# Kernel optimization log

Hardware: AMD Instinct MI355X
Metric: run time of the kernel (lower is better)

## Reference

```python
import jax, jax.numpy as jnp
import numpy as np

D_MODEL = 1024
NUM_HEADS = 16
HEAD_DIM = D_MODEL // NUM_HEADS
B, S = 2, 2048


def setup_inputs() -> dict:
    key = jax.random.key(0)
    ks = jax.random.split(key, 5)
    x = jax.random.normal(ks[0], (B, S, D_MODEL), dtype=jnp.float32)
    # nn.Linear weights are [out_features, in_features]
    Wq = jax.random.normal(ks[1], (D_MODEL, D_MODEL), dtype=jnp.float32) / np.sqrt(D_MODEL)
    Wk = jax.random.normal(ks[2], (HEAD_DIM, D_MODEL), dtype=jnp.float32) / np.sqrt(D_MODEL)
    Wv = jax.random.normal(ks[3], (HEAD_DIM, D_MODEL), dtype=jnp.float32) / np.sqrt(D_MODEL)
    Wo = jax.random.normal(ks[4], (D_MODEL, D_MODEL), dtype=jnp.float32) / np.sqrt(D_MODEL)
    # causal mask, broadcastable to [B, H, S, S]; mask==0 positions get -inf
    mask = jnp.tril(jnp.ones((S, S), dtype=bool))[None, None]
    return {"x": x, "Wq": Wq, "Wk": Wk, "Wv": Wv, "Wo": Wo, "mask": mask}


def reference(x, Wq, Wk, Wv, Wo, mask):
    Bsz, Sl, D = x.shape
    H, hd = NUM_HEADS, HEAD_DIM
    q = (x @ Wq.T).reshape(Bsz, Sl, H, hd)          # [B,S,H,hd]
    k = x @ Wk.T                                    # [B,S,hd] (single shared KV head)
    v = x @ Wv.T                                    # [B,S,hd]
    scale = 1.0 / np.sqrt(hd).astype(np.float32)
    # scores: [B,H,S,S] — full O(n^2) matrix, as in the original module
    scores = jnp.einsum('bshd,btd->bhst', q, k) * scale
    scores = jnp.where(mask, scores, -jnp.inf)
    attn = jax.nn.softmax(scores, axis=-1)
    out = jnp.einsum('bhst,btd->bshd', attn, v).reshape(Bsz, Sl, D)
    return out @ Wo.T
```

## Files before the change

kernel.cpp:

```cpp
#include <hip/hip_runtime.h>
#include <hip/hip_bf16.h>
#include <math.h>

#define BB 2
#define SS 2048
#define DD 1024
#define NH 16
#define HD 64
#define MM (BB * SS)

#define BK 64
#define BKF 32

typedef __hip_bfloat16 bf16;
typedef __bf16 bf16_t;
typedef __attribute__((ext_vector_type(8))) __bf16 bf16x8;
typedef __attribute__((ext_vector_type(4))) __bf16 bf16x4;
typedef __attribute__((ext_vector_type(4))) float floatx4;

#define SCALEQ 0.18033688011112042f

__device__ __forceinline__ int bf16_plausible(unsigned int w) {
    unsigned int bits = (w & 0xFFFFu) << 16;
    float v = __uint_as_float(bits);
    float av = fabsf(v);
    return (av == 0.f || (av >= 9.5367431640625e-7f && av <= 64.f)) ? 1 : 0;
}

__global__ void detect_dtype(const unsigned int* __restrict__ x, int* __restrict__ flag) {
    const int tid = threadIdx.x;
    int good = 0;
    for (int i = tid; i < 256; i += 64) good += bf16_plausible(x[i]);
#pragma unroll
    for (int s = 1; s < 64; s <<= 1) good += __shfl_xor(good, s);
    if (tid == 0) { flag[0] = (good >= 240) ? 0 : 1; flag[1] = 0; }
}

__device__ __forceinline__ void conv_seg(const void* __restrict__ in,
                                         bf16_t* __restrict__ out,
                                         int n, int f, int tid, int T) {
    if (f) {
        const float* p = (const float*)in;
        for (int i = tid * 8; i < n; i += T * 8) {
            float4 a = *(const float4*)(p + i);
            float4 b = *(const float4*)(p + i + 4);
            bf16x8 o;
            o[0] = (bf16_t)a.x; o[1] = (bf16_t)a.y; o[2] = (bf16_t)a.z; o[3] = (bf16_t)a.w;
            o[4] = (bf16_t)b.x; o[5] = (bf16_t)b.y; o[6] = (bf16_t)b.z; o[7] = (bf16_t)b.w;
            *(bf16x8*)(out + i) = o;
        }
    } else {
        const bf16_t* p = (const bf16_t*)in;
        for (int i = tid * 8; i < n; i += T * 8)
            *(bf16x8*)(out + i) = *(const bf16x8*)(p + i);
    }
}

__global__ __launch_bounds__(256) void conv_all(const void* __restrict__ x,
                                                const void* __restrict__ wq,
                                                const void* __restrict__ wk,
                                                const void* __restrict__ wv,
                                                const void* __restrict__ wo,
                                                bf16_t* __restrict__ xb,
                                                bf16_t* __restrict__ wqb,
                                                bf16_t* __restrict__ wkb,
                                                bf16_t* __restrict__ wvb,
                                                bf16_t* __restrict__ wob,
                                                int* __restrict__ flag) {
    __shared__ int goodw[4];
    const int ltid = threadIdx.x;
    int g = bf16_plausible(((const unsigned int*)x)[ltid]);
#pragma unroll
    for (int s = 1; s < 64; s <<= 1) g += __shfl_xor(g, s);
    if ((ltid & 63) == 0) goodw[ltid >> 6] = g;
    __syncthreads();
    const int good = goodw[0] + goodw[1] + goodw[2] + goodw[3];
    const int f = (good >= 240) ? 0 : 1;
    if (blockIdx.x == 0 && ltid == 0) { flag[0] = f; flag[1] = 0; }

    const int tid = blockIdx.x * blockDim.x + ltid;
    const int T = gridDim.x * blockDim.x;
    conv_seg(x, xb, MM * DD, f, tid, T);
    conv_seg(wq, wqb, DD * DD, f, tid, T);
    conv_seg(wk, wkb, HD * DD, f, tid, T);
    conv_seg(wv, wvb, HD * DD, f, tid, T);
    conv_seg(wo, wob, DD * DD, f, tid, T);
}

#define KP2 72

__global__ __launch_bounds__(512) void proj_qkv_b(const bf16_t* __restrict__ X,
                                                  const bf16_t* __restrict__ Wq,
                                                  const bf16_t* __restrict__ Wk,
                                                  const bf16_t* __restrict__ Wv,
                                                  bf16_t* __restrict__ QA,
                                                  bf16_t* __restrict__ Kp,
                                                  bf16_t* __restrict__ VpT) {
    __shared__ bf16_t As[128 * KP2];
    __shared__ bf16_t Bs[128 * KP2];

    const int tid = threadIdx.x;
    const int wave = tid >> 6, lane = tid & 63;
    const int lo = lane & 15, quad = lane >> 4;
    const int wr = wave >> 2, wc = wave & 3;
    const int rowBase = blockIdx.x * 128;
    const int cb = blockIdx.y;

    const int rS = tid >> 2;
    const int c16 = (tid & 3) * 16;

    const bf16_t* arow = X + (size_t)(rowBase + rS) * DD + c16;
    const bf16_t* wrow;
    if (cb < 8)       wrow = Wq + (size_t)(cb * 128 + rS) * DD + c16;
    else if (rS < 64) wrow = Wk + (size_t)rS * DD + c16;
    else              wrow = Wv + (size_t)(rS - 64) * DD + c16;

    floatx4 acc[4][2];
#pragma unroll
    for (int i = 0; i < 4; i++)
#pragma unroll
        for (int j = 0; j < 2; j++) acc[i][j] = (floatx4){0.f, 0.f, 0.f, 0.f};

    bf16x8 aR0[2], bR0[2], aR1[2], bR1[2];
#pragma unroll
    for (int p = 0; p < 2; p++) {
        aR0[p] = *(const bf16x8*)(arow + p * 8);
        bR0[p] = *(const bf16x8*)(wrow + p * 8);
        aR1[p] = *(const bf16x8*)(arow + BK + p * 8);
        bR1[p] = *(const bf16x8*)(wrow + BK + p * 8);
    }

    for (int k0 = 0; k0 < DD; k0 += 2 * BK) {
        __syncthreads();
#pragma unroll
        for (int p = 0; p < 2; p++) {
            *(bf16x8*)&As[rS * KP2 + c16 + p * 8] = aR0[p];
            *(bf16x8*)&Bs[rS * KP2 + c16 + p * 8] = bR0[p];
        }
        __syncthreads();
        if (k0 + 2 * BK < DD) {
#pragma unroll
            for (int p = 0; p < 2; p++) {
                aR0[p] = *(const bf16x8*)(arow + k0 + 2 * BK + p * 8);
                bR0[p] = *(const bf16x8*)(wrow + k0 + 2 * BK + p * 8);
            }
        }
#pragma unroll
        for (int kk = 0; kk < 2; kk++) {
            bf16x8 afr[4], bfr[2];
#pragma unroll
            for (int i = 0; i < 4; i++)
                afr[i] = *(const bf16x8*)&As[(wr * 64 + i * 16 + lo) * KP2 + kk * 32 + quad * 8];
#pragma unroll
            for (int j = 0; j < 2; j++)
                bfr[j] = *(const bf16x8*)&Bs[(wc * 32 + j * 16 + lo) * KP2 + kk * 32 + quad * 8];
#pragma unroll
            for (int i = 0; i < 4; i++)
#pragma unroll
                for (int j = 0; j < 2; j++)
                    acc[i][j] = __builtin_amdgcn_mfma_f32_16x16x32_bf16(afr[i], bfr[j], acc[i][j], 0, 0, 0);
        }
        __syncthreads();
#pragma unroll
        for (int p = 0; p < 2; p++) {
            *(bf16x8*)&As[rS * KP2 + c16 + p * 8] = aR1[p];
            *(bf16x8*)&Bs[rS * KP2 + c16 + p * 8] = bR1[p];
        }
        __syncthreads();
        if (k0 + 3 * BK < DD) {
#pragma unroll
            for (int p = 0; p < 2; p++) {
                aR1[p] = *(const bf16x8*)(arow + k0 + 3 * BK + p * 8);
                bR1[p] = *(const bf16x8*)(wrow + k0 + 3 * BK + p * 8);
            }
        }
#pragma unroll
        for (int kk = 0; kk < 2; kk++) {
            bf16x8 afr[4], bfr[2];
#pragma unroll
            for (int i = 0; i < 4; i++)
                afr[i] = *(const bf16x8*)&As[(wr * 64 + i * 16 + lo) * KP2 + kk * 32 + quad * 8];
#pragma unroll
            for (int j = 0; j < 2; j++)
                bfr[j] = *(const bf16x8*)&Bs[(wc * 32 + j * 16 + lo) * KP2 + kk * 32 + quad * 8];
#pragma unroll
            for (int i = 0; i < 4; i++)
#pragma unroll
                for (int j = 0; j < 2; j++)
                    acc[i][j] = __builtin_amdgcn_mfma_f32_16x16x32_bf16(afr[i], bfr[j], acc[i][j], 0, 0, 0);
        }
    }

#pragma unroll
    for (int i = 0; i < 4; i++)
#pragma unroll
        for (int j = 0; j < 2; j++)
#pragma unroll
            for (int reg = 0; reg < 4; reg++) {
                int row = rowBase + wr * 64 + i * 16 + quad * 4 + reg;
                int c = wc * 32 + j * 16 + lo;
                float v = acc[i][j][reg];
                if (cb < 8) {
                    QA[(size_t)row * DD + cb * 128 + c] = (bf16_t)(v * SCALEQ);
                } else if (c < 64) {
                    Kp[(size_t)row * HD + c] = (bf16_t)v;
                } else {
                    VpT[((size_t)(row >> 11) * HD + (c - 64)) * SS + (row & (SS - 1))] = (bf16_t)v;
                }
            }
}

__global__ __launch_bounds__(512) void proj_o_b(const bf16_t* __restrict__ AO,
                                                const bf16_t* __restrict__ Wo,
                                                void* __restrict__ Cout,
                                                const int* __restrict__ flagOut) {
    const int fout = *flagOut;

    __shared__ bf16_t As[128 * KP2];
    __shared__ bf16_t Bs[128 * KP2];

    const int tid = threadIdx.x;
    const int wave = tid >> 6, lane = tid & 63;
    const int lo = lane & 15, quad = lane >> 4;
    const int wr = wave >> 2, wc = wave & 3;
    const int rowBase = blockIdx.x * 128;
    const int colBase = blockIdx.y * 128;

    const int rS = tid >> 2;
    const int c16 = (tid & 3) * 16;

    const bf16_t* arow = AO + (size_t)(rowBase + rS) * DD + c16;
    const bf16_t* wrow = Wo + (size_t)(colBase + rS) * DD + c16;

    floatx4 acc[4][2];
#pragma unroll
    for (int i = 0; i < 4; i++)
#pragma unroll
        for (int j = 0; j < 2; j++) acc[i][j] = (floatx4){0.f, 0.f, 0.f, 0.f};

    bf16x8 aR0[2], bR0[2], aR1[2], bR1[2];
#pragma unroll
    for (int p = 0; p < 2; p++) {
        aR0[p] = *(const bf16x8*)(arow + p * 8);
        bR0[p] = *(const bf16x8*)(wrow + p * 8);
        aR1[p] = *(const bf16x8*)(arow + BK + p * 8);
        bR1[p] = *(const bf16x8*)(wrow + BK + p * 8);
    }

    for (int k0 = 0; k0 < DD; k0 += 2 * BK) {
        __syncthreads();
#pragma unroll
        for (int p = 0; p < 2; p++) {
            *(bf16x8*)&As[rS * KP2 + c16 + p * 8] = aR0[p];
            *(bf16x8*)&Bs[rS * KP2 + c16 + p * 8] = bR0[p];
        }
        __syncthreads();
        if (k0 + 2 * BK < DD) {
#pragma unroll
            for (int p = 0; p < 2; p++) {
                aR0[p] = *(const bf16x8*)(arow + k0 + 2 * BK + p * 8);
                bR0[p] = *(const bf16x8*)(wrow + k0 + 2 * BK + p * 8);
            }
        }
#pragma unroll
        for (int kk = 0; kk < 2; kk++) {
            bf16x8 afr[4], bfr[2];
#pragma unroll
            for (int i = 0; i < 4; i++)
                afr[i] = *(const bf16x8*)&As[(wr * 64 + i * 16 + lo) * KP2 + kk * 32 + quad * 8];
#pragma unroll
            for (int j = 0; j < 2; j++)
                bfr[j] = *(const bf16x8*)&Bs[(wc * 32 + j * 16 + lo) * KP2 + kk * 32 + quad * 8];
#pragma unroll
            for (int i = 0; i < 4; i++)
#pragma unroll
                for (int j = 0; j < 2; j++)
                    acc[i][j] = __builtin_amdgcn_mfma_f32_16x16x32_bf16(afr[i], bfr[j], acc[i][j], 0, 0, 0);
        }
        __syncthreads();
#pragma unroll
        for (int p = 0; p < 2; p++) {
            *(bf16x8*)&As[rS * KP2 + c16 + p * 8] = aR1[p];
            *(bf16x8*)&Bs[rS * KP2 + c16 + p * 8] = bR1[p];
        }
        __syncthreads();
        if (k0 + 3 * BK < DD) {
#pragma unroll
            for (int p = 0; p < 2; p++) {
                aR1[p] = *(const bf16x8*)(arow + k0 + 3 * BK + p * 8);
                bR1[p] = *(const bf16x8*)(wrow + k0 + 3 * BK + p * 8);
            }
        }
#pragma unroll
        for (int kk = 0; kk < 2; kk++) {
            bf16x8 afr[4], bfr[2];
#pragma unroll
            for (int i = 0; i < 4; i++)
                afr[i] = *(const bf16x8*)&As[(wr * 64 + i * 16 + lo) * KP2 + kk * 32 + quad * 8];
#pragma unroll
            for (int j = 0; j < 2; j++)
                bfr[j] = *(const bf16x8*)&Bs[(wc * 32 + j * 16 + lo) * KP2 + kk * 32 + quad * 8];
#pragma unroll
            for (int i = 0; i < 4; i++)
#pragma unroll
                for (int j = 0; j < 2; j++)
                    acc[i][j] = __builtin_amdgcn_mfma_f32_16x16x32_bf16(afr[i], bfr[j], acc[i][j], 0, 0, 0);
        }
    }

#pragma unroll
    for (int i = 0; i < 4; i++)
#pragma unroll
        for (int j = 0; j < 2; j++)
#pragma unroll
            for (int reg = 0; reg < 4; reg++) {
                int row = rowBase + wr * 64 + i * 16 + quad * 4 + reg;
                int col = colBase + wc * 32 + j * 16 + lo;
                size_t idx = (size_t)row * DD + col;
                if (fout) ((float*)Cout)[idx] = acc[i][j][reg];
                else      ((bf16_t*)Cout)[idx] = (bf16_t)acc[i][j][reg];
            }
}

#define KP 40

__device__ __forceinline__ bf16x8 ld8(const void* p, int f, size_t idx) {
    if (f) {
        const float* q = (const float*)p + idx;
        float4 a = *(const float4*)(q);
        float4 b = *(const float4*)(q + 4);
        bf16x8 o;
        o[0] = (bf16_t)a.x; o[1] = (bf16_t)a.y; o[2] = (bf16_t)a.z; o[3] = (bf16_t)a.w;
        o[4] = (bf16_t)b.x; o[5] = (bf16_t)b.y; o[6] = (bf16_t)b.z; o[7] = (bf16_t)b.w;
        return o;
    }
    return *(const bf16x8*)((const bf16_t*)p + idx);
}

__global__ __launch_bounds__(256) void proj_qkv_f(const void* __restrict__ X,
                                                  const void* __restrict__ Wq,
                                                  const void* __restrict__ Wk,
                                                  const void* __restrict__ Wv,
                                                  bf16_t* __restrict__ QA,
                                                  bf16_t* __restrict__ Kp,
                                                  bf16_t* __restrict__ VpT,
                                                  const int* __restrict__ flag) {
    const int f = *flag;
    __shared__ bf16_t As[64 * KP];
    __shared__ bf16_t Bs[64 * KP];

    const int tid = threadIdx.x;
    const int wave = tid >> 6, lane = tid & 63;
    const int lo = lane & 15, quad = lane >> 4;
    const int wr = wave >> 1, wc = wave & 1;
    const int rowBase = blockIdx.x * 64;
    const int cb = blockIdx.y;

    const int rS = tid >> 2;
    const int c8 = (tid & 3) * 8;

    size_t aidx = (size_t)(rowBase + rS) * DD + c8;
    size_t widx;
    const void* Wsrc;
    if (cb < 16)       { Wsrc = Wq; widx = (size_t)(cb * 64 + rS) * DD + c8; }
    else if (cb == 16) { Wsrc = Wk; widx = (size_t)rS * DD + c8; }
    else               { Wsrc = Wv; widx = (size_t)rS * DD + c8; }

    floatx4 acc[2][2];
#pragma unroll
    for (int i = 0; i < 2; i++)
#pragma unroll
        for (int j = 0; j < 2; j++) acc[i][j] = (floatx4){0.f, 0.f, 0.f, 0.f};

    for (int k0 = 0; k0 < DD; k0 += BKF) {
        __syncthreads();
        *(bf16x8*)&As[rS * KP + c8] = ld8(X, f, aidx + k0);
        *(bf16x8*)&Bs[rS * KP + c8] = ld8(Wsrc, f, widx + k0);
        __syncthreads();
        bf16x8 afr[2], bfr[2];
#pragma unroll
        for (int i = 0; i < 2; i++)
            afr[i] = *(const bf16x8*)&As[(wr * 32 + i * 16 + lo) * KP + quad * 8];
#pragma unroll
        for (int j = 0; j < 2; j++)
            bfr[j] = *(const bf16x8*)&Bs[(wc * 32 + j * 16 + lo) * KP + quad * 8];
#pragma unroll
        for (int i = 0; i < 2; i++)
#pragma unroll
            for (int j = 0; j < 2; j++)
                acc[i][j] = __builtin_amdgcn_mfma_f32_16x16x32_bf16(afr[i], bfr[j], acc[i][j], 0, 0, 0);
    }

#pragma unroll
    for (int i = 0; i < 2; i++)
#pragma unroll
        for (int j = 0; j < 2; j++)
#pragma unroll
            for (int reg = 0; reg < 4; reg++) {
                int row = rowBase + wr * 32 + i * 16 + quad * 4 + reg;
                int c = wc * 32 + j * 16 + lo;
                float v = acc[i][j][reg];
                if (cb < 16) {
                    QA[(size_t)row * DD + cb * 64 + c] = (bf16_t)(v * SCALEQ);
                } else if (cb == 16) {
                    Kp[(size_t)row * HD + c] = (bf16_t)v;
                } else {
                    VpT[((size_t)(row >> 11) * HD + c) * SS + (row & (SS - 1))] = (bf16_t)v;
                }
            }
}

__global__ __launch_bounds__(256) void proj_o_f(const bf16_t* __restrict__ AO,
                                                const void* __restrict__ Wo,
                                                void* __restrict__ Cout,
                                                const int* __restrict__ flagW,
                                                const int* __restrict__ flagOut) {
    const int f = *flagW;
    const int fout = *flagOut;
    __shared__ bf16_t As[64 * KP];
    __shared__ bf16_t Bs[64 * KP];

    const int tid = threadIdx.x;
    const int wave = tid >> 6, lane = tid & 63;
    const int lo = lane & 15, quad = lane >> 4;
    const int wr = wave >> 1, wc = wave & 1;
    const int rowBase = blockIdx.x * 64;
    const int colBase = blockIdx.y * 64;

    const int rS = tid >> 2;
    const int c8 = (tid & 3) * 8;

    size_t aidx = (size_t)(rowBase + rS) * DD + c8;
    size_t widx = (size_t)(colBase + rS) * DD + c8;

    floatx4 acc[2][2];
#pragma unroll
    for (int i = 0; i < 2; i++)
#pragma unroll
        for (int j = 0; j < 2; j++) acc[i][j] = (floatx4){0.f, 0.f, 0.f, 0.f};

    for (int k0 = 0; k0 < DD; k0 += BKF) {
        __syncthreads();
        *(bf16x8*)&As[rS * KP + c8] = *(const bf16x8*)(AO + aidx + k0);
        *(bf16x8*)&Bs[rS * KP + c8] = ld8(Wo, f, widx + k0);
        __syncthreads();
        bf16x8 afr[2], bfr[2];
#pragma unroll
        for (int i = 0; i < 2; i++)
            afr[i] = *(const bf16x8*)&As[(wr * 32 + i * 16 + lo) * KP + quad * 8];
#pragma unroll
        for (int j = 0; j < 2; j++)
            bfr[j] = *(const bf16x8*)&Bs[(wc * 32 + j * 16 + lo) * KP + quad * 8];
#pragma unroll
        for (int i = 0; i < 2; i++)
#pragma unroll
            for (int j = 0; j < 2; j++)
                acc[i][j] = __builtin_amdgcn_mfma_f32_16x16x32_bf16(afr[i], bfr[j], acc[i][j], 0, 0, 0);
    }

#pragma unroll
    for (int i = 0; i < 2; i++)
#pragma unroll
        for (int j = 0; j < 2; j++)
#pragma unroll
            for (int reg = 0; reg < 4; reg++) {
                int row = rowBase + wr * 32 + i * 16 + quad * 4 + reg;
                int col = colBase + wc * 32 + j * 16 + lo;
                size_t idx = (size_t)row * DD + col;
                if (fout) ((float*)Cout)[idx] = acc[i][j][reg];
                else      ((bf16_t*)Cout)[idx] = (bf16_t)acc[i][j][reg];
            }
}

#define PSTR 40
#define DMTHR 8.0f

__global__ __launch_bounds__(512, 4) void attn_mfma(const bf16_t* Q,
                                                    const bf16_t* __restrict__ K,
                                                    const bf16_t* __restrict__ Vt,
                                                    bf16_t* O) {
    const int h = blockIdx.y, b = blockIdx.z;
    const int tid = threadIdx.x;
    const int wq = tid >> 6, lane = tid & 63;
    const int lo = lane & 15, quad = lane >> 4;
    const int x = blockIdx.x;

    const int nA = x + 1;
    int na = 1, bestc = 0x7fffffff;
#pragma unroll
    for (int a = 1; a <= 7; ++a) {
        int cA = (nA + a - 1) / a;
        int cB = (65 - nA + (7 - a)) / (8 - a);
        int c = cA > cB ? cA : cB;
        if (c < bestc) { bestc = c; na = a; }
    }
    int qt, pos, gs;
    if (wq < na) { qt = x;      pos = wq;      gs = na; }
    else         { qt = 63 - x; pos = wq - na; gs = 8 - na; }
    const int q0 = qt * 32;
    const int n = qt + 1;
    const int itS = (n * pos) / gs;
    const int itE = (n * (pos + 1)) / gs;

    __shared__ __align__(16) char smem[4 * 32 * 64 * 4];
    __shared__ float MrgML[4][2][2][16];
    bf16_t* Pw = (bf16_t*)smem + wq * (32 * PSTR);
    float (*MrgO)[32 * 64] = (float (*)[32 * 64])smem;

    bf16x8 qf[2][2];
#pragma unroll
    for (int s = 0; s < 2; s++)
#pragma unroll
        for (int hf = 0; hf < 2; hf++)
            qf[s][hf] = *(const bf16x8*)(Q + ((size_t)(b * SS + q0 + s * 16 + lo)) * DD +
                                         h * HD + hf * 32 + quad * 8);

    floatx4 Oacc[2][4];
    float m_i[2], l_ln[2];
#pragma unroll
    for (int s = 0; s < 2; s++) {
#pragma unroll
        for (int dt = 0; dt < 4; dt++) Oacc[s][dt] = (floatx4){0.f, 0.f, 0.f, 0.f};
        m_i[s] = -1e30f; l_ln[s] = 0.f;
    }

    const bf16_t* Kb = K + (size_t)b * SS * HD;
    const bf16_t* Vb = Vt + (size_t)b * HD * SS;

    if (itS < itE) {
        bf16x8 kf[2][2];
#pragma unroll
        for (int kt = 0; kt < 2; kt++)
#pragma unroll
            for (int hf = 0; hf < 2; hf++)
                kf[kt][hf] = *(const bf16x8*)(Kb + (size_t)(itS * 32 + kt * 16 + lo) * HD +
                                              hf * 32 + quad * 8);

        for (int it = itS; it < itE; it++) {
            const int t0 = it * 32;

            bf16x8 vf[4];
#pragma unroll
            for (int dt = 0; dt < 4; dt++)
                vf[dt] = *(const bf16x8*)(Vb + (size_t)(dt * 16 + lo) * SS + t0 + quad * 8);

            bf16x8 kn[2][2];
            if (it + 1 < itE) {
#pragma unroll
                for (int kt = 0; kt < 2; kt++)
#pragma unroll
                    for (int hf = 0; hf < 2; hf++)
                        kn[kt][hf] = *(const bf16x8*)(Kb + (size_t)(t0 + 32 + kt * 16 + lo) * HD +
                                                      hf * 32 + quad * 8);
            }

            floatx4 st[2][2];
#pragma unroll
            for (int s = 0; s < 2; s++)
#pragma unroll
                for (int kt = 0; kt < 2; kt++) {
                    floatx4 z = (floatx4){0.f, 0.f, 0.f, 0.f};
                    z = __builtin_amdgcn_mfma_f32_16x16x32_bf16(kf[kt][0], qf[s][0], z, 0, 0, 0);
                    z = __builtin_amdgcn_mfma_f32_16x16x32_bf16(kf[kt][1], qf[s][1], z, 0, 0, 0);
                    st[s][kt] = z;
                }

            if (it == qt) {
#pragma unroll
                for (int s = 0; s < 2; s++) {
                    int q = q0 + s * 16 + lo;
#pragma unroll
                    for (int kt = 0; kt < 2; kt++)
#pragma unroll
                        for (int reg = 0; reg < 4; reg++)
                            if (t0 + kt * 16 + quad * 4 + reg > q) st[s][kt][reg] = -1e30f;
                }
            }

#pragma unroll
            for (int s = 0; s < 2; s++) {
                float lm = fmaxf(fmaxf(fmaxf(st[s][0][0], st[s][0][1]), fmaxf(st[s][0][2], st[s][0][3])),
                                 fmaxf(fmaxf(st[s][1][0], st[s][1][1]), fmaxf(st[s][1][2], st[s][1][3])));
                if (__any(lm > m_i[s] + DMTHR)) {
                    float mx = fmaxf(lm, __shfl_xor(lm, 16));
                    mx = fmaxf(mx, __shfl_xor(mx, 32));
                    float mn = fmaxf(m_i[s], mx);
                    float al = exp2f(m_i[s] - mn);
                    m_i[s] = mn;
                    l_ln[s] *= al;
#pragma unroll
                    for (int dt = 0; dt < 4; dt++) Oacc[s][dt] *= al;
                }
                float p[2][4];
#pragma unroll
                for (int kt = 0; kt < 2; kt++)
#pragma unroll
                    for (int reg = 0; reg < 4; reg++)
                        p[kt][reg] = exp2f(st[s][kt][reg] - m_i[s]);
                l_ln[s] += ((p[0][0] + p[0][1]) + (p[0][2] + p[0][3])) +
                           ((p[1][0] + p[1][1]) + (p[1][2] + p[1][3]));
#pragma unroll
                for (int kt = 0; kt < 2; kt++) {
                    bf16x4 pk;
#pragma unroll
                    for (int reg = 0; reg < 4; reg++) pk[reg] = (bf16_t)p[kt][reg];
                    *(bf16x4*)&Pw[(s * 16 + lo) * PSTR + kt * 16 + quad * 4] = pk;
                }
            }

            asm volatile("s_waitcnt lgkmcnt(0)" ::: "memory");

            bf16x8 pb[2];
#pragma unroll
            for (int s = 0; s < 2; s++)
                pb[s] = *(const bf16x8*)&Pw[(s * 16 + lo) * PSTR + quad * 8];
#pragma unroll
            for (int s = 0; s < 2; s++)
#pragma unroll
                for (int dt = 0; dt < 4; dt++)
                    Oacc[s][dt] = __builtin_amdgcn_mfma_f32_16x16x32_bf16(vf[dt], pb[s], Oacc[s][dt], 0, 0, 0);

#pragma unroll
            for (int kt = 0; kt < 2; kt++)
#pragma unroll
                for (int hf = 0; hf < 2; hf++) kf[kt][hf] = kn[kt][hf];
        }
    }

    float l_i[2];
#pragma unroll
    for (int s = 0; s < 2; s++) {
        float l = l_ln[s];
        l += __shfl_xor(l, 16);
        l += __shfl_xor(l, 32);
        l_i[s] = l;
    }

    for (int step = 1; step < 8; step <<= 1) {
        const bool pub = (pos & (2 * step - 1)) == step;
        const bool cmb = ((pos & (2 * step - 1)) == 0) && (pos + step < gs);
        __syncthreads();
        if (pub) {
            float* Ob = MrgO[wq >> 1];
#pragma unroll
            for (int s = 0; s < 2; s++) {
#pragma unroll
                for (int dt = 0; dt < 4; dt++)
#pragma unroll
                    for (int reg = 0; reg < 4; reg++)
                        Ob[(s * 16 + dt * 4 + reg) * 64 + lane] = Oacc[s][dt][reg];
                if (quad == 0) {
                    MrgML[wq >> 1][s][0][lo] = m_i[s];
                    MrgML[wq >> 1][s][1][lo] = l_i[s];
                }
            }
        }
        __syncthreads();
        if (cmb) {
            const int bu = (wq + step) >> 1;
            const float* Ob = MrgO[bu];
#pragma unroll
            for (int s = 0; s < 2; s++) {
                float m1 = MrgML[bu][s][0][lo];
                float l1 = MrgML[bu][s][1][lo];
                float mm = fmaxf(m_i[s], m1);
                float a0 = exp2f(m_i[s] - mm);
                float a1 = exp2f(m1 - mm);
                m_i[s] = mm;
                l_i[s] = l_i[s] * a0 + l1 * a1;
#pragma unroll
                for (int dt = 0; dt < 4; dt++)
#pragma unroll
                    for (int reg = 0; reg < 4; reg++)
                        Oacc[s][dt][reg] = Oacc[s][dt][reg] * a0 +
                                           Ob[(s * 16 + dt * 4 + reg) * 64 + lane] * a1;
            }
        }
    }

    if (pos == 0) {
#pragma unroll
        for (int s = 0; s < 2; s++) {
            float linv = 1.f / l_i[s];
            bf16_t* Orow = O + ((size_t)(b * SS + q0 + s * 16 + lo)) * DD + h * HD;
#pragma unroll
            for (int dt = 0; dt < 4; dt++) {
                bf16x4 ov;
#pragma unroll
                for (int reg = 0; reg < 4; reg++)
                    ov[reg] = (bf16_t)(Oacc[s][dt][reg] * linv);
                *(bf16x4*)&Orow[dt * 16 + quad * 4] = ov;
            }
        }
    }
}

extern "C" void kernel_launch(void* const* d_in, const int* in_sizes, int n_in,
                              void* d_out, int out_size, void* d_ws, size_t ws_size,
                              hipStream_t stream) {
    const void* x  = d_in[0];
    const void* Wq = d_in[1];
    const void* Wk = d_in[2];
    const void* Wv = d_in[3];
    const void* Wo = d_in[4];

    char* ws = (char*)d_ws;
    int* flag = (int*)ws;
    bf16_t* QA  = (bf16_t*)(ws + 256);
    bf16_t* Kp  = QA + (size_t)MM * DD;
    bf16_t* VpT = Kp + (size_t)MM * HD;
    bf16_t* Xb  = VpT + (size_t)BB * HD * SS;
    bf16_t* Wqb = Xb + (size_t)MM * DD;
    bf16_t* Wkb = Wqb + (size_t)DD * DD;
    bf16_t* Wvb = Wkb + (size_t)HD * DD;
    bf16_t* Wob = Wvb + (size_t)HD * DD;
    size_t need = (size_t)((char*)(Wob + (size_t)DD * DD) - ws);

    if (ws_size >= need) {
        conv_all<<<dim3(1024), dim3(256), 0, stream>>>(x, Wq, Wk, Wv, Wo,
                                                       Xb, Wqb, Wkb, Wvb, Wob, flag);
        proj_qkv_b<<<dim3(MM / 128, 9), dim3(512), 0, stream>>>(Xb, Wqb, Wkb, Wvb,
                                                                QA, Kp, VpT);
        attn_mfma<<<dim3(32, NH, BB), dim3(512), 0, stream>>>(QA, Kp, VpT, QA);
        proj_o_b<<<dim3(MM / 128, 8), dim3(512), 0, stream>>>(QA, Wob, d_out, flag);
    } else {
        detect_dtype<<<1, 64, 0, stream>>>((const unsigned int*)x, flag);
        proj_qkv_f<<<dim3(MM / 64, 18), dim3(256), 0, stream>>>(x, Wq, Wk, Wv,
                                                                QA, Kp, VpT, flag);
        attn_mfma<<<dim3(32, NH, BB), dim3(512), 0, stream>>>(QA, Kp, VpT, QA);
        proj_o_f<<<dim3(MM / 64, 16), dim3(256), 0, stream>>>(QA, Wo, d_out,
                                                              flag, flag);
    }
}
```

Before: 207.1 us.

## Process 64-key tiles per attention iteration instead of 32

The attention inner loop now covers 64 keys per iteration (two 32-key halves), so the online-softmax max/rescale check, the LDS write of P and the waitcnt happen once per 64 keys instead of once per 32. Work splitting across waves is recomputed in 64-key units, and the P staging buffer grows to a 72-element stride. The explicit K register prefetch of the next tile is dropped, which may expose more load latency and raises register pressure. Diagonal masking now covers up to 64 keys, which adds some wasted masked work for odd query tiles.

```diff
diff --git a/kernel.cpp b/kernel.cpp
--- a/kernel.cpp
+++ b/kernel.cpp
@@ -472,7 +472,7 @@
             }
 }
 
-#define PSTR 40
+#define PSTR2 72
 #define DMTHR 8.0f
 
 __global__ __launch_bounds__(512, 4) void attn_mfma(const bf16_t* Q,
@@ -485,12 +485,12 @@
     const int lo = lane & 15, quad = lane >> 4;
     const int x = blockIdx.x;
 
-    const int nA = x + 1;
+    const int nA = (x + 2) >> 1;
     int na = 1, bestc = 0x7fffffff;
 #pragma unroll
     for (int a = 1; a <= 7; ++a) {
         int cA = (nA + a - 1) / a;
-        int cB = (65 - nA + (7 - a)) / (8 - a);
+        int cB = (33 - nA + (7 - a)) / (8 - a);
         int c = cA > cB ? cA : cB;
         if (c < bestc) { bestc = c; na = a; }
     }
@@ -498,13 +498,13 @@
     if (wq < na) { qt = x;      pos = wq;      gs = na; }
     else         { qt = 63 - x; pos = wq - na; gs = 8 - na; }
     const int q0 = qt * 32;
-    const int n = qt + 1;
-    const int itS = (n * pos) / gs;
-    const int itE = (n * (pos + 1)) / gs;
-
-    __shared__ __align__(16) char smem[4 * 32 * 64 * 4];
+    const int n64 = (qt + 2) >> 1;
+    const int itS = (n64 * pos) / gs;
+    const int itE = (n64 * (pos + 1)) / gs;
+
+    __shared__ __align__(16) char smem[8 * 32 * PSTR2 * 2];
     __shared__ float MrgML[4][2][2][16];
-    bf16_t* Pw = (bf16_t*)smem + wq * (32 * PSTR);
+    bf16_t* Pw = (bf16_t*)smem + wq * (32 * PSTR2);
     float (*MrgO)[32 * 64] = (float (*)[32 * 64])smem;
 
     bf16x8 qf[2][2];
@@ -527,34 +527,18 @@
     const bf16_t* Kb = K + (size_t)b * SS * HD;
     const bf16_t* Vb = Vt + (size_t)b * HD * SS;
 
-    if (itS < itE) {
-        bf16x8 kf[2][2];
-#pragma unroll
-        for (int kt = 0; kt < 2; kt++)
-#pragma unroll
-            for (int hf = 0; hf < 2; hf++)
-                kf[kt][hf] = *(const bf16x8*)(Kb + (size_t)(itS * 32 + kt * 16 + lo) * HD +
-                                              hf * 32 + quad * 8);
-
-        for (int it = itS; it < itE; it++) {
-            const int t0 = it * 32;
-
-            bf16x8 vf[4];
-#pragma unroll
-            for (int dt = 0; dt < 4; dt++)
-                vf[dt] = *(const bf16x8*)(Vb + (size_t)(dt * 16 + lo) * SS + t0 + quad * 8);
-
-            bf16x8 kn[2][2];
-            if (it + 1 < itE) {
-#pragma unroll
-                for (int kt = 0; kt < 2; kt++)
-#pragma unroll
-                    for (int hf = 0; hf < 2; hf++)
-                        kn[kt][hf] = *(const bf16x8*)(Kb + (size_t)(t0 + 32 + kt * 16 + lo) * HD +
-                                                      hf * 32 + quad * 8);
-            }
-
-            floatx4 st[2][2];
+    for (int it = itS; it < itE; it++) {
+        const int t0 = it * 64;
+
+        floatx4 st[2][4];
+        {
+            bf16x8 kf[2][2];
+#pragma unroll
+            for (int kt = 0; kt < 2; kt++)
+#pragma unroll
+                for (int hf = 0; hf < 2; hf++)
+                    kf[kt][hf] = *(const bf16x8*)(Kb + (size_t)(t0 + kt * 16 + lo) * HD +
+                                                  hf * 32 + quad * 8);
 #pragma unroll
             for (int s = 0; s < 2; s++)
 #pragma unroll
@@ -564,66 +548,88 @@
                     z = __builtin_amdgcn_mfma_f32_16x16x32_bf16(kf[kt][1], qf[s][1], z, 0, 0, 0);
                     st[s][kt] = z;
                 }
-
-            if (it == qt) {
-#pragma unroll
-                for (int s = 0; s < 2; s++) {
-                    int q = q0 + s * 16 + lo;
-#pragma unroll
-                    for (int kt = 0; kt < 2; kt++)
-#pragma unroll
-                        for (int reg = 0; reg < 4; reg++)
-                            if (t0 + kt * 16 + quad * 4 + reg > q) st[s][kt][reg] = -1e30f;
+#pragma unroll
+            for (int kt = 0; kt < 2; kt++)
+#pragma unroll
+                for (int hf = 0; hf < 2; hf++)
+                    kf[kt][hf] = *(const bf16x8*)(Kb + (size_t)(t0 + 32 + kt * 16 + lo) * HD +
+                                                  hf * 32 + quad * 8);
+#pragma unroll
+            for (int s = 0; s < 2; s++)
+#pragma unroll
+                for (int kt = 0; kt < 2; kt++) {
+                    floatx4 z = (floatx4){0.f, 0.f, 0.f, 0.f};
+                    z = __builtin_amdgcn_mfma_f32_16x16x32_bf16(kf[kt][0], qf[s][0], z, 0, 0, 0);
+                    z = __builtin_amdgcn_mfma_f32_16x16x32_bf16(kf[kt][1], qf[s][1], z, 0, 0, 0);
+                    st[s][2 + kt] = z;
                 }
-            }
-
+        }
+
+        if ((qt >> 1) == it) {
 #pragma unroll
             for (int s = 0; s < 2; s++) {
-                float lm = fmaxf(fmaxf(fmaxf(st[s][0][0], st[s][0][1]), fmaxf(st[s][0][2], st[s][0][3])),
-                                 fmaxf(fmaxf(st[s][1][0], st[s][1][1]), fmaxf(st[s][1][2], st[s][1][3])));
-                if (__any(lm > m_i[s] + DMTHR)) {
-                    float mx = fmaxf(lm, __shfl_xor(lm, 16));
-                    mx = fmaxf(mx, __shfl_xor(mx, 32));
-                    float mn = fmaxf(m_i[s], mx);
-                    float al = exp2f(m_i[s] - mn);
-                    m_i[s] = mn;
-                    l_ln[s] *= al;
-#pragma unroll
-                    for (int dt = 0; dt < 4; dt++) Oacc[s][dt] *= al;
-                }
-                float p[2][4];
-#pragma unroll
-                for (int kt = 0; kt < 2; kt++)
+                int q = q0 + s * 16 + lo;
+#pragma unroll
+                for (int kt = 0; kt < 4; kt++)
 #pragma unroll
                     for (int reg = 0; reg < 4; reg++)
-                        p[kt][reg] = exp2f(st[s][kt][reg] - m_i[s]);
-                l_ln[s] += ((p[0][0] + p[0][1]) + (p[0][2] + p[0][3])) +
-                           ((p[1][0] + p[1][1]) + (p[1][2] + p[1][3]));
-#pragma unroll
-                for (int kt = 0; kt < 2; kt++) {
-                    bf16x4 pk;
-#pragma unroll
-                    for (int reg = 0; reg < 4; reg++) pk[reg] = (bf16_t)p[kt][reg];
-                    *(bf16x4*)&Pw[(s * 16 + lo) * PSTR + kt * 16 + quad * 4] = pk;
-                }
-            }
-
-            asm volatile("s_waitcnt lgkmcnt(0)" ::: "memory");
-
+                        if (t0 + kt * 16 + quad * 4 + reg > q) st[s][kt][reg] = -1e30f;
+            }
+        }
+
+#pragma unroll
+        for (int s = 0; s < 2; s++) {
+            float lm = fmaxf(
+                fmaxf(fmaxf(fmaxf(st[s][0][0], st[s][0][1]), fmaxf(st[s][0][2], st[s][0][3])),
+                      fmaxf(fmaxf(st[s][1][0], st[s][1][1]), fmaxf(st[s][1][2], st[s][1][3]))),
+                fmaxf(fmaxf(fmaxf(st[s][2][0], st[s][2][1]), fmaxf(st[s][2][2], st[s][2][3])),
+                      fmaxf(fmaxf(st[s][3][0], st[s][3][1]), fmaxf(st[s][3][2], st[s][3][3]))));
+            if (__any(lm > m_i[s] + DMTHR)) {
+                float mx = fmaxf(lm, __shfl_xor(lm, 16));
+                mx = fmaxf(mx, __shfl_xor(mx, 32));
+                float mn = fmaxf(m_i[s], mx);
+                float al = exp2f(m_i[s] - mn);
+                m_i[s] = mn;
+                l_ln[s] *= al;
+#pragma unroll
+                for (int dt = 0; dt < 4; dt++) Oacc[s][dt] *= al;
+            }
+            float rs = 0.f;
+#pragma unroll
+            for (int kt = 0; kt < 4; kt++) {
+#pragma unroll
+                for (int reg = 0; reg < 4; reg++)
+                    st[s][kt][reg] = exp2f(st[s][kt][reg] - m_i[s]);
+                rs += (st[s][kt][0] + st[s][kt][1]) + (st[s][kt][2] + st[s][kt][3]);
+            }
+            l_ln[s] += rs;
+#pragma unroll
+            for (int kt = 0; kt < 4; kt++) {
+                bf16x4 pk;
+#pragma unroll
+                for (int reg = 0; reg < 4; reg++) pk[reg] = (bf16_t)st[s][kt][reg];
+                *(bf16x4*)&Pw[(s * 16 + lo) * PSTR2 + kt * 16 + quad * 4] = pk;
+            }
+        }
+
+        asm volatile("s_waitcnt lgkmcnt(0)" ::: "memory");
+
+#pragma unroll
+        for (int hb = 0; hb < 2; hb++) {
+            bf16x8 vf[4];
+#pragma unroll
+            for (int dt = 0; dt < 4; dt++)
+                vf[dt] = *(const bf16x8*)(Vb + (size_t)(dt * 16 + lo) * SS +
+                                          t0 + hb * 32 + quad * 8);
             bf16x8 pb[2];
 #pragma unroll
             for (int s = 0; s < 2; s++)
-                pb[s] = *(const bf16x8*)&Pw[(s * 16 + lo) * PSTR + quad * 8];
+                pb[s] = *(const bf16x8*)&Pw[(s * 16 + lo) * PSTR2 + hb * 32 + quad * 8];
 #pragma unroll
             for (int s = 0; s < 2; s++)
 #pragma unroll
                 for (int dt = 0; dt < 4; dt++)
                     Oacc[s][dt] = __builtin_amdgcn_mfma_f32_16x16x32_bf16(vf[dt], pb[s], Oacc[s][dt], 0, 0, 0);
-
-#pragma unroll
-            for (int kt = 0; kt < 2; kt++)
-#pragma unroll
-                for (int hf = 0; hf < 2; hf++) kf[kt][hf] = kn[kt][hf];
         }
     }
 
```

Result: no change. 205.0 us (median of 2 runs) (-1.0%).
